# Performance work log

Hardware: AMD Instinct MI355X
Metric: run time of the kernel (lower is better)

Reference implementation:

```python
import jax, jax.numpy as jnp
import numpy as np

N_NODES = 50000
BN_EPS = 1e-5


def graph_conv(x, row, col, ew, n):
    # deg from source indices only (matches torch.bincount(row))
    deg = jnp.zeros((n,), x.dtype).at[row].add(1.0)
    dinv = jnp.where(deg > 0, deg ** -0.5, 0.0)
    norm = dinv[row] * ew * dinv[col]                     # [E]
    msg = norm[:, None] * x[row]                          # [E, F]
    return jax.ops.segment_sum(msg, col, num_segments=n)  # out[dst] += w * x[src]


def batch_norm(x, gamma, beta):
    # training-mode BN over the node (batch) dim, biased variance
    mu = jnp.mean(x, axis=0)
    var = jnp.mean((x - mu) ** 2, axis=0)
    return (x - mu) / jnp.sqrt(var + BN_EPS) * gamma + beta


def setup_inputs() -> dict:
    key = jax.random.key(0)
    ks = jax.random.split(key, 12)
    node_features = jax.random.normal(ks[0], (N_NODES, 100), dtype=jnp.float32)
    edge_index = jax.random.randint(ks[1], (2, 800000), 0, N_NODES, dtype=jnp.int64)
    edge_weights = jax.random.uniform(ks[2], (800000,), dtype=jnp.float32)
    def lin(k, fi, fo):
        lim = 1.0 / np.sqrt(fi)
        k1, k2 = jax.random.split(k)
        W = jax.random.uniform(k1, (fi, fo), minval=-lim, maxval=lim, dtype=jnp.float32)
        b = jax.random.uniform(k2, (fo,), minval=-lim, maxval=lim, dtype=jnp.float32)
        return W, b
    W0, b0 = lin(ks[3], 100, 128)
    W1, b1 = lin(ks[4], 128, 128)
    W2, b2 = lin(ks[5], 128, 64)
    return {
        "node_features": node_features, "edge_index": edge_index, "edge_weights": edge_weights,
        "W0": W0, "b0": b0, "g0": jnp.ones((128,), jnp.float32), "be0": jnp.zeros((128,), jnp.float32),
        "W1": W1, "b1": b1, "g1": jnp.ones((128,), jnp.float32), "be1": jnp.zeros((128,), jnp.float32),
        "W2": W2, "b2": b2,
    }


def reference(node_features, edge_index, edge_weights,
              W0, b0, g0, be0, W1, b1, g1, be1, W2, b2):
    n = node_features.shape[0]
    row, col = edge_index[0], edge_index[1]
    x = node_features
    # layer 0
    x = graph_conv(x, row, col, edge_weights, n)
    x = jax.nn.relu(batch_norm(x @ W0 + b0, g0, be0))
    # layer 1
    x = graph_conv(x, row, col, edge_weights, n)
    x = jax.nn.relu(batch_norm(x @ W1 + b1, g1, be1))
    # final layer (no BN/relu)
    x = graph_conv(x, row, col, edge_weights, n)
    return x @ W2 + b2
```

## Files before the change

### kernel.cpp

```cpp
#include <hip/hip_runtime.h>
#include <cstdint>

#define F0 100
#define FH 128
#define FO 64
#define PD 4
#define BN_EPS 1e-5f

typedef unsigned short ushort_t;
typedef unsigned int uint_t;

static inline int ceil_div(long long a, long long b) { return (int)((a + b - 1) / b); }

__device__ __forceinline__ float bf_lo(uint_t w) { return __uint_as_float(w << 16); }
__device__ __forceinline__ float bf_hi(uint_t w) { return __uint_as_float(w & 0xffff0000u); }
__device__ __forceinline__ uint_t f2bf(float f) {
  uint_t u = __float_as_uint(f);
  return (u + 0x7fffu + ((u >> 16) & 1u)) >> 16;
}
__device__ __forceinline__ uint_t pack2(float a, float b) {
  return f2bf(a) | (f2bf(b) << 16);
}


template <int K, int F, int TM, int BK, bool A_BF16, bool OUT_BF16>
__device__ __forceinline__ void gemm2_body(int bid, const void* __restrict__ A_,
                                           const float* __restrict__ W,
                                           const float* __restrict__ bias,
                                           void* __restrict__ out_, int n) {
  constexpr int NCG = F / 4;
  constexpr int NRG = 256 / NCG;
  constexpr int BR = NRG * TM;
  constexpr int F4 = F / 4;

  __shared__ float sW[BK][F];
  __shared__ float sA[BR][BK];

  const int tid = threadIdx.x;
  const int cg = tid % NCG;
  const int rg = tid / NCG;
  const int row0 = bid * BR;

  float4 acc[TM];
#pragma unroll
  for (int t = 0; t < TM; ++t) acc[t] = make_float4(0.f, 0.f, 0.f, 0.f);

  const float4* W4 = (const float4*)W;
  const float4 z4 = make_float4(0.f, 0.f, 0.f, 0.f);

  for (int k0 = 0; k0 < K; k0 += BK) {
    for (int i = tid; i < BK * F4; i += 256) {
      int kk = i / F4, f4 = i % F4;
      int gk = k0 + kk;
      ((float4*)&sW[kk][0])[f4] = (gk < K) ? W4[(size_t)gk * F4 + f4] : z4;
    }
    for (int i = tid; i < BR * (BK / 4); i += 256) {
      int r = i / (BK / 4), k4 = i % (BK / 4);
      int gr = row0 + r;
      int gk = k0 + k4 * 4;
      float4 av = z4;
      if (gr < n && gk + 3 < K) {
        if (A_BF16) {
          uint2 u = ((const uint2*)A_)[(size_t)gr * (K / 4) + (gk >> 2)];
          av.x = bf_lo(u.x); av.y = bf_hi(u.x);
          av.z = bf_lo(u.y); av.w = bf_hi(u.y);
        } else {
          av = ((const float4*)A_)[(size_t)gr * (K / 4) + (gk >> 2)];
        }
      }
      ((float4*)&sA[r][0])[k4] = av;
    }
    __syncthreads();
#pragma unroll 4
    for (int kk = 0; kk < BK; ++kk) {
      float4 w = ((const float4*)&sW[kk][0])[cg];
#pragma unroll
      for (int t = 0; t < TM; ++t) {
        float a = sA[rg * TM + t][kk];
        acc[t].x = fmaf(a, w.x, acc[t].x);
        acc[t].y = fmaf(a, w.y, acc[t].y);
        acc[t].z = fmaf(a, w.z, acc[t].z);
        acc[t].w = fmaf(a, w.w, acc[t].w);
      }
    }
    __syncthreads();
  }

  float4 bb = bias ? ((const float4*)bias)[cg] : z4;
#pragma unroll
  for (int t = 0; t < TM; ++t) {
    int gr = row0 + rg * TM + t;
    if (gr < n) {
      float4 v = acc[t];
      v.x += bb.x; v.y += bb.y; v.z += bb.z; v.w += bb.w;
      if (OUT_BF16) {
        ((uint2*)out_)[(size_t)gr * F4 + cg] = make_uint2(pack2(v.x, v.y), pack2(v.z, v.w));
      } else {
        ((float4*)out_)[(size_t)gr * F4 + cg] = v;
      }
    }
  }
}


__global__ __launch_bounds__(256) void fused_gemm_hist_kernel(
    const float* __restrict__ A, const float* __restrict__ W, void* __restrict__ out, int n,
    int GB, const int* __restrict__ row, const int* __restrict__ col,
    int* __restrict__ degr_p, int* __restrict__ degc_p, int* __restrict__ posw, int E) {
  int bid = blockIdx.x;
  int r5 = bid % 5;
  int g = bid / 5;
  if (r5 == 0 && g < GB) {
    gemm2_body<F0, FH, 8, 16, false, true>(g, A, W, nullptr, out, n);
    return;
  }
  int h = (r5 == 0) ? (bid - GB) : (bid - (g + 1));
  int e = h * 256 + threadIdx.x;
  if (e >= E) return;
  atomicAdd(&degr_p[(size_t)row[e] * PD], 1);
  posw[e] = atomicAdd(&degc_p[(size_t)col[e] * PD], 1);
}


__global__ __launch_bounds__(256) void scan_fused_kernel(const int* __restrict__ degr_p,
                                                         const int* __restrict__ degc_p,
                                                         float* __restrict__ dinv,
                                                         int* __restrict__ startp,
                                                         int* __restrict__ bsums, int n) {
  __shared__ int s[256];
  int i = blockIdx.x * 256 + threadIdx.x;
  int dc = 0;
  if (i < n) {
    int dr = degr_p[(size_t)i * PD];
    dc = degc_p[(size_t)i * PD];
    dinv[i] = (dr > 0) ? rsqrtf((float)dr) : 0.0f;
  }
  s[threadIdx.x] = dc;
  __syncthreads();
  for (int off = 1; off < 256; off <<= 1) {
    int t = 0;
    if (threadIdx.x >= off) t = s[threadIdx.x - off];
    __syncthreads();
    if (threadIdx.x >= off) s[threadIdx.x] += t;
    __syncthreads();
  }
  if (i < n) startp[i] = s[threadIdx.x] - dc;
  if (threadIdx.x == 255) bsums[blockIdx.x] = s[255];
}

__global__ __launch_bounds__(256) void scan_partials_kernel(int* __restrict__ bsums, int nb) {
  __shared__ int s[256];
  int v = (threadIdx.x < nb) ? bsums[threadIdx.x] : 0;
  s[threadIdx.x] = v;
  __syncthreads();
  for (int off = 1; off < 256; off <<= 1) {
    int t = 0;
    if (threadIdx.x >= off) t = s[threadIdx.x - off];
    __syncthreads();
    if (threadIdx.x >= off) s[threadIdx.x] += t;
    __syncthreads();
  }
  if (threadIdx.x < nb) bsums[threadIdx.x] = s[threadIdx.x] - v;
}


__global__ __launch_bounds__(256) void csr_scatter2_kernel(const int* __restrict__ row,
                                                           const int* __restrict__ col,
                                                           const float* __restrict__ ew,
                                                           const float* __restrict__ dinv,
                                                           const int* __restrict__ startp,
                                                           const int* __restrict__ bsums,
                                                           const int* __restrict__ posw,
                                                           int2* __restrict__ ep, int E) {
  int e = blockIdx.x * blockDim.x + threadIdx.x;
  if (e >= E) return;
  int r = row[e], c = col[e];
  int pos = startp[c] + bsums[c >> 8] + posw[e];
  float coef = dinv[r] * ew[e] * dinv[c];
  ep[pos] = make_int2(r, __float_as_int(coef));
}


template <bool DO_BN>
__device__ __forceinline__ void conv_accum_128(const ushort_t* __restrict__ x, int s0, int d,
                                               int q, const int2* __restrict__ ep,
                                               const float* __restrict__ scale,
                                               const float* __restrict__ shift,
                                               float* __restrict__ acc) {
  constexpr int G2 = FH / 8;
  constexpr int TPD = 8;
  const uint4* x4 = (const uint4*)x;

  float sc[16], sh[16];
  if (DO_BN) {
#pragma unroll
    for (int ch = 0; ch < 2; ++ch) {
      int g = q + ch * TPD;
#pragma unroll
      for (int j = 0; j < 8; ++j) {
        sc[ch * 8 + j] = scale[g * 8 + j];
        sh[ch * 8 + j] = shift[g * 8 + j];
      }
    }
  }
#pragma unroll
  for (int j = 0; j < 16; ++j) acc[j] = 0.f;

  for (int k = 0; k < d; ++k) {
    int2 e = ep[s0 + k];
    float c = __int_as_float(e.y);
    const uint4* xp = x4 + (size_t)e.x * G2 + q;
    uint4 v0 = xp[0];
    uint4 v1 = xp[TPD];
    uint_t vv[8] = {v0.x, v0.y, v0.z, v0.w, v1.x, v1.y, v1.z, v1.w};
#pragma unroll
    for (int hh = 0; hh < 8; ++hh) {
      float f0 = bf_lo(vv[hh]);
      float f1 = bf_hi(vv[hh]);
      if (DO_BN) {
        f0 = fmaxf(fmaf(f0, sc[2 * hh], sh[2 * hh]), 0.f);
        f1 = fmaxf(fmaf(f1, sc[2 * hh + 1], sh[2 * hh + 1]), 0.f);
      }
      acc[2 * hh] = fmaf(c, f0, acc[2 * hh]);
      acc[2 * hh + 1] = fmaf(c, f1, acc[2 * hh + 1]);
    }
  }
}


__global__ __launch_bounds__(256) void conv0_kernel(const ushort_t* __restrict__ x,
                                                    const int* __restrict__ startp,
                                                    const int* __restrict__ bsums,
                                                    const int* __restrict__ degc_p,
                                                    const int2* __restrict__ ep,
                                                    const float* __restrict__ bias,
                                                    ushort_t* __restrict__ out, int n) {
  constexpr int TPD = 8;
  long long tid = (long long)blockIdx.x * 256 + threadIdx.x;
  if (tid >= (long long)n * TPD) return;
  int dst = (int)(tid / TPD);
  int q = (int)(tid % TPD);
  int s0 = startp[dst] + bsums[dst >> 8];
  int d = degc_p[(size_t)dst * PD];
  float acc[16];
  conv_accum_128<false>(x, s0, d, q, ep, nullptr, nullptr, acc);
#pragma unroll
  for (int ch = 0; ch < 2; ++ch) {
    int g = q + ch * TPD;
#pragma unroll
    for (int j = 0; j < 8; ++j) acc[ch * 8 + j] += bias[g * 8 + j];
  }
  uint4* o4 = (uint4*)out;
  size_t base = (size_t)dst * (FH / 8);
  o4[base + q] = make_uint4(pack2(acc[0], acc[1]), pack2(acc[2], acc[3]),
                            pack2(acc[4], acc[5]), pack2(acc[6], acc[7]));
  o4[base + q + TPD] = make_uint4(pack2(acc[8], acc[9]), pack2(acc[10], acc[11]),
                                  pack2(acc[12], acc[13]), pack2(acc[14], acc[15]));
}


template <int FOUT, bool OUT_F32>
__global__ __launch_bounds__(256) void convgemm_kernel(const ushort_t* __restrict__ x,
                                                       const int* __restrict__ startp,
                                                       const int* __restrict__ bsums,
                                                       const int* __restrict__ degc_p,
                                                       const int2* __restrict__ ep,
                                                       const float* __restrict__ scale,
                                                       const float* __restrict__ shift,
                                                       const float* __restrict__ W,
                                                       const float* __restrict__ bias,
                                                       void* __restrict__ out, int n) {
  constexpr int TPD = 8;
  constexpr int BKG = 16;
  constexpr int CPT = FOUT / 8;
  __shared__ float sY[32][FH + 1];
  __shared__ float sW[BKG][FOUT];

  const int tid = threadIdx.x;
  const int dl = tid / TPD;
  const int q = tid % TPD;
  const int dst = blockIdx.x * 32 + dl;
  const bool valid = dst < n;

  float acc[16];
  if (valid) {
    int s0 = startp[dst] + bsums[dst >> 8];
    int d = degc_p[(size_t)dst * PD];
    conv_accum_128<true>(x, s0, d, q, ep, scale, shift, acc);
  } else {
#pragma unroll
    for (int j = 0; j < 16; ++j) acc[j] = 0.f;
  }
#pragma unroll
  for (int j = 0; j < 8; ++j) {
    sY[dl][8 * q + j] = acc[j];
    sY[dl][64 + 8 * q + j] = acc[8 + j];
  }
  __syncthreads();

  const int r = tid / 8;
  const int cg = tid % 8;
  float oacc[CPT];
#pragma unroll
  for (int j = 0; j < CPT; ++j) oacc[j] = 0.f;

  const float4* W4 = (const float4*)W;
  for (int k0 = 0; k0 < FH; k0 += BKG) {
    for (int i = tid; i < BKG * (FOUT / 4); i += 256) {
      int kk = i / (FOUT / 4), f4 = i % (FOUT / 4);
      ((float4*)&sW[kk][0])[f4] = W4[(size_t)(k0 + kk) * (FOUT / 4) + f4];
    }
    __syncthreads();
#pragma unroll 4
    for (int kk = 0; kk < BKG; ++kk) {
      float a = sY[r][k0 + kk];
      const float* wrow = &sW[kk][cg * CPT];
#pragma unroll
      for (int j = 0; j < CPT; ++j) oacc[j] = fmaf(a, wrow[j], oacc[j]);
    }
    __syncthreads();
  }

  int gr = blockIdx.x * 32 + r;
  if (gr >= n) return;
#pragma unroll
  for (int j = 0; j < CPT; ++j) oacc[j] += bias[cg * CPT + j];

  if (OUT_F32) {
    float4* o4 = (float4*)out;
    size_t base = (size_t)gr * (FOUT / 4) + cg * (CPT / 4);
#pragma unroll
    for (int j = 0; j < CPT / 4; ++j)
      o4[base + j] = make_float4(oacc[4 * j], oacc[4 * j + 1], oacc[4 * j + 2], oacc[4 * j + 3]);
  } else {
    uint2* o2 = (uint2*)out;
    size_t base = (size_t)gr * (FOUT / 4) + cg * (CPT / 4);
#pragma unroll
    for (int j = 0; j < CPT / 4; ++j)
      o2[base + j] = make_uint2(pack2(oacc[4 * j], oacc[4 * j + 1]),
                                pack2(oacc[4 * j + 2], oacc[4 * j + 3]));
  }
}


__global__ __launch_bounds__(128) void bn_stats_fin_kernel(const ushort_t* __restrict__ z,
                                                           float* __restrict__ sum,
                                                           float* __restrict__ sumsq,
                                                           const float* __restrict__ g,
                                                           const float* __restrict__ be,
                                                           float* __restrict__ scale,
                                                           float* __restrict__ shift,
                                                           int n, int* __restrict__ ctr) {
  int f = threadIdx.x;
  float s = 0.0f, s2 = 0.0f;
  for (int r = blockIdx.x; r < n; r += gridDim.x) {
    float v = __uint_as_float(((uint_t)z[(size_t)r * FH + f]) << 16);
    s += v;
    s2 += v * v;
  }
  unsafeAtomicAdd(&sum[f], s);
  unsafeAtomicAdd(&sumsq[f], s2);
  __threadfence();
  __syncthreads();
  __shared__ int lastFlag;
  if (f == 0) lastFlag = (atomicAdd(ctr, 1) == (int)gridDim.x - 1) ? 1 : 0;
  __syncthreads();
  if (lastFlag) {
    float S = atomicAdd(&sum[f], 0.0f);
    float S2 = atomicAdd(&sumsq[f], 0.0f);
    float invN = 1.0f / (float)n;
    float mean = S * invN;
    float var = fmaxf(S2 * invN - mean * mean, 0.0f);
    float sc = g[f] / sqrtf(var + BN_EPS);
    scale[f] = sc;
    shift[f] = be[f] - mean * sc;
  }
}


extern "C" void kernel_launch(void* const* d_in, const int* in_sizes, int n_in,
                              void* d_out, int out_size, void* d_ws, size_t ws_size,
                              hipStream_t stream) {
  const float* x   = (const float*)d_in[0];
  const int*   ei  = (const int*)d_in[1];
  const float* ew  = (const float*)d_in[2];
  const float* W0  = (const float*)d_in[3];
  const float* b0  = (const float*)d_in[4];
  const float* g0  = (const float*)d_in[5];
  const float* be0 = (const float*)d_in[6];
  const float* W1  = (const float*)d_in[7];
  const float* b1  = (const float*)d_in[8];
  const float* g1  = (const float*)d_in[9];
  const float* be1 = (const float*)d_in[10];
  const float* W2  = (const float*)d_in[11];
  const float* b2  = (const float*)d_in[12];

  const int n = in_sizes[0] / F0;
  const int E = in_sizes[2];
  const int* row = ei;
  const int* col = ei + E;

  ushort_t* bufA  = (ushort_t*)d_ws;
  ushort_t* bufB  = bufA + (size_t)n * FH;
  int2*   ep      = (int2*)(bufB + (size_t)n * FH);
  int*    degc_p  = (int*)(ep + E);
  int*    degr_p  = degc_p + (size_t)n * PD;
  float*  sum0    = (float*)(degr_p + (size_t)n * PD);
  float*  sumsq0  = sum0 + FH;
  float*  sum1    = sumsq0 + FH;
  float*  sumsq1  = sum1 + FH;
  int*    ctr     = (int*)(sumsq1 + FH);
  const size_t zero_bytes = (2 * (size_t)n * PD + 4 * FH + 2) * 4;
  int*    startp  = ctr + 2;
  float*  dinv    = (float*)(startp + n);
  int*    bsums   = (int*)(dinv + n);
  float*  scale0  = (float*)(bsums + 256);
  float*  shift0  = scale0 + FH;
  float*  scale1  = shift0 + FH;
  float*  shift1  = scale1 + FH;
  int*    posw    = (int*)bufB;

  const int nb = ceil_div(n, 256);
  const int GB = ceil_div(n, 64);
  const int HB = ceil_div(E, 256);
  const int CB = ceil_div(n, 32);

  (void)hipMemsetAsync(degc_p, 0, zero_bytes, stream);
  fused_gemm_hist_kernel<<<GB + HB, 256, 0, stream>>>(x, W0, bufA, n, GB, row, col,
                                                      degr_p, degc_p, posw, E);
  scan_fused_kernel<<<nb, 256, 0, stream>>>(degr_p, degc_p, dinv, startp, bsums, n);
  scan_partials_kernel<<<1, 256, 0, stream>>>(bsums, nb);
  csr_scatter2_kernel<<<HB, 256, 0, stream>>>(row, col, ew, dinv, startp, bsums, posw, ep, E);

  conv0_kernel<<<CB, 256, 0, stream>>>(bufA, startp, bsums, degc_p, ep, b0, bufB, n);
  bn_stats_fin_kernel<<<256, 128, 0, stream>>>(bufB, sum0, sumsq0, g0, be0, scale0, shift0,
                                               n, ctr + 0);
  convgemm_kernel<FH, false><<<CB, 256, 0, stream>>>(bufB, startp, bsums, degc_p, ep,
                                                     scale0, shift0, W1, b1, bufA, n);
  bn_stats_fin_kernel<<<256, 128, 0, stream>>>(bufA, sum1, sumsq1, g1, be1, scale1, shift1,
                                               n, ctr + 1);
  convgemm_kernel<FO, true><<<CB, 256, 0, stream>>>(bufA, startp, bsums, degc_p, ep,
                                                    scale1, shift1, W2, b2, (float*)d_out, n);
}
```

Before: 409.7 us.

## Unfuse conv+GEMM, reorder final layer to GEMM-then-conv, fuse scan passes

The fused conv+GEMM kernels are split into a standalone CSR aggregation kernel and a tiled GEMM kernel. The last layer now applies W2 before aggregation, so it gathers 64-wide rows instead of 128-wide ones, with the BN1 scale/shift and ReLU folded into the GEMM's A-tile load. The separate scan-partials kernel is folded into the scan kernel using a last-block counter, and BN statistics now use 16-byte loads with a shared-memory reduction. This adds launches and bf16 intermediate round trips through memory in exchange for cheaper gathers and better GEMM tiling. The extra bf16 rounding of the intermediates is a precision risk.

```diff
diff --git a/kernel.cpp b/kernel.cpp
--- a/kernel.cpp
+++ b/kernel.cpp
@@ -23,10 +23,12 @@
 }
 
 
-template <int K, int F, int TM, int BK, bool A_BF16, bool OUT_BF16>
+template <int K, int F, int TM, int BK, bool BN_A, bool A_BF16, bool OUT_BF16>
 __device__ __forceinline__ void gemm2_body(int bid, const void* __restrict__ A_,
                                            const float* __restrict__ W,
                                            const float* __restrict__ bias,
+                                           const float* __restrict__ scA,
+                                           const float* __restrict__ shA,
                                            void* __restrict__ out_, int n) {
   constexpr int NCG = F / 4;
   constexpr int NRG = 256 / NCG;
@@ -67,6 +69,14 @@
         } else {
           av = ((const float4*)A_)[(size_t)gr * (K / 4) + (gk >> 2)];
         }
+        if (BN_A) {
+          float4 sc = ((const float4*)scA)[gk >> 2];
+          float4 sh = ((const float4*)shA)[gk >> 2];
+          av.x = fmaxf(fmaf(av.x, sc.x, sh.x), 0.f);
+          av.y = fmaxf(fmaf(av.y, sc.y, sh.y), 0.f);
+          av.z = fmaxf(fmaf(av.z, sc.z, sh.z), 0.f);
+          av.w = fmaxf(fmaf(av.w, sc.w, sh.w), 0.f);
+        }
       }
       ((float4*)&sA[r][0])[k4] = av;
     }
@@ -102,6 +112,16 @@
   }
 }
 
+template <int K, int F, int TM, int BK, bool BN_A, bool A_BF16, bool OUT_BF16>
+__global__ __launch_bounds__(256) void gemm2_kernel(const void* __restrict__ A,
+                                                    const float* __restrict__ W,
+                                                    const float* __restrict__ bias,
+                                                    const float* __restrict__ scA,
+                                                    const float* __restrict__ shA,
+                                                    void* __restrict__ out, int n) {
+  gemm2_body<K, F, TM, BK, BN_A, A_BF16, OUT_BF16>(blockIdx.x, A, W, bias, scA, shA, out, n);
+}
+
 
 __global__ __launch_bounds__(256) void fused_gemm_hist_kernel(
     const float* __restrict__ A, const float* __restrict__ W, void* __restrict__ out, int n,
@@ -111,7 +131,7 @@
   int r5 = bid % 5;
   int g = bid / 5;
   if (r5 == 0 && g < GB) {
-    gemm2_body<F0, FH, 8, 16, false, true>(g, A, W, nullptr, out, n);
+    gemm2_body<F0, FH, 8, 16, false, false, true>(g, A, W, nullptr, nullptr, nullptr, out, n);
     return;
   }
   int h = (r5 == 0) ? (bid - GB) : (bid - (g + 1));
@@ -126,41 +146,46 @@
                                                          const int* __restrict__ degc_p,
                                                          float* __restrict__ dinv,
                                                          int* __restrict__ startp,
-                                                         int* __restrict__ bsums, int n) {
+                                                         int* __restrict__ bsums, int n,
+                                                         int* __restrict__ ctr) {
   __shared__ int s[256];
-  int i = blockIdx.x * 256 + threadIdx.x;
+  const int tid = threadIdx.x;
+  int i = blockIdx.x * 256 + tid;
   int dc = 0;
   if (i < n) {
     int dr = degr_p[(size_t)i * PD];
     dc = degc_p[(size_t)i * PD];
     dinv[i] = (dr > 0) ? rsqrtf((float)dr) : 0.0f;
   }
-  s[threadIdx.x] = dc;
+  s[tid] = dc;
   __syncthreads();
   for (int off = 1; off < 256; off <<= 1) {
     int t = 0;
-    if (threadIdx.x >= off) t = s[threadIdx.x - off];
-    __syncthreads();
-    if (threadIdx.x >= off) s[threadIdx.x] += t;
-    __syncthreads();
-  }
-  if (i < n) startp[i] = s[threadIdx.x] - dc;
-  if (threadIdx.x == 255) bsums[blockIdx.x] = s[255];
-}
-
-__global__ __launch_bounds__(256) void scan_partials_kernel(int* __restrict__ bsums, int nb) {
-  __shared__ int s[256];
-  int v = (threadIdx.x < nb) ? bsums[threadIdx.x] : 0;
-  s[threadIdx.x] = v;
+    if (tid >= off) t = s[tid - off];
+    __syncthreads();
+    if (tid >= off) s[tid] += t;
+    __syncthreads();
+  }
+  if (i < n) startp[i] = s[tid] - dc;
+  if (tid == 255) bsums[blockIdx.x] = s[255];
+  __threadfence();
+  __syncthreads();
+  __shared__ int lastFlag;
+  if (tid == 0) lastFlag = (atomicAdd(ctr, 1) == (int)gridDim.x - 1) ? 1 : 0;
+  __syncthreads();
+  if (!lastFlag) return;
+  int nb = (int)gridDim.x;
+  int v = (tid < nb) ? atomicAdd(&bsums[tid], 0) : 0;
+  s[tid] = v;
   __syncthreads();
   for (int off = 1; off < 256; off <<= 1) {
     int t = 0;
-    if (threadIdx.x >= off) t = s[threadIdx.x - off];
-    __syncthreads();
-    if (threadIdx.x >= off) s[threadIdx.x] += t;
-    __syncthreads();
-  }
-  if (threadIdx.x < nb) bsums[threadIdx.x] = s[threadIdx.x] - v;
+    if (tid >= off) t = s[tid - off];
+    __syncthreads();
+    if (tid >= off) s[tid] += t;
+    __syncthreads();
+  }
+  if (tid < nb) bsums[tid] = s[tid] - v;
 }
 
 
@@ -181,14 +206,24 @@
 }
 
 
-template <bool DO_BN>
-__device__ __forceinline__ void conv_accum_128(const ushort_t* __restrict__ x, int s0, int d,
-                                               int q, const int2* __restrict__ ep,
-                                               const float* __restrict__ scale,
-                                               const float* __restrict__ shift,
-                                               float* __restrict__ acc) {
-  constexpr int G2 = FH / 8;
-  constexpr int TPD = 8;
+template <int F, bool DO_BN, bool OUT_F32>
+__global__ __launch_bounds__(256) void conv_kernel(const ushort_t* __restrict__ x,
+                                                   const int* __restrict__ startp,
+                                                   const int* __restrict__ bsums,
+                                                   const int* __restrict__ degc_p,
+                                                   const int2* __restrict__ ep,
+                                                   const float* __restrict__ bias,
+                                                   const float* __restrict__ scale,
+                                                   const float* __restrict__ shift,
+                                                   void* __restrict__ out, int n) {
+  constexpr int G2 = F / 8;
+  constexpr int TPD = G2 / 2;
+  long long tid = (long long)blockIdx.x * 256 + threadIdx.x;
+  if (tid >= (long long)n * TPD) return;
+  int dst = (int)(tid / TPD);
+  int q = (int)(tid % TPD);
+  int s0 = startp[dst] + bsums[dst >> 8];
+  int d = degc_p[(size_t)dst * PD];
   const uint4* x4 = (const uint4*)x;
 
   float sc[16], sh[16];
@@ -203,6 +238,8 @@
       }
     }
   }
+
+  float acc[16];
 #pragma unroll
   for (int j = 0; j < 16; ++j) acc[j] = 0.f;
 
@@ -225,155 +262,107 @@
       acc[2 * hh + 1] = fmaf(c, f1, acc[2 * hh + 1]);
     }
   }
-}
-
-
-__global__ __launch_bounds__(256) void conv0_kernel(const ushort_t* __restrict__ x,
-                                                    const int* __restrict__ startp,
-                                                    const int* __restrict__ bsums,
-                                                    const int* __restrict__ degc_p,
-                                                    const int2* __restrict__ ep,
-                                                    const float* __restrict__ bias,
-                                                    ushort_t* __restrict__ out, int n) {
-  constexpr int TPD = 8;
-  long long tid = (long long)blockIdx.x * 256 + threadIdx.x;
-  if (tid >= (long long)n * TPD) return;
-  int dst = (int)(tid / TPD);
-  int q = (int)(tid % TPD);
-  int s0 = startp[dst] + bsums[dst >> 8];
-  int d = degc_p[(size_t)dst * PD];
-  float acc[16];
-  conv_accum_128<false>(x, s0, d, q, ep, nullptr, nullptr, acc);
-#pragma unroll
-  for (int ch = 0; ch < 2; ++ch) {
-    int g = q + ch * TPD;
-#pragma unroll
-    for (int j = 0; j < 8; ++j) acc[ch * 8 + j] += bias[g * 8 + j];
-  }
-  uint4* o4 = (uint4*)out;
-  size_t base = (size_t)dst * (FH / 8);
-  o4[base + q] = make_uint4(pack2(acc[0], acc[1]), pack2(acc[2], acc[3]),
-                            pack2(acc[4], acc[5]), pack2(acc[6], acc[7]));
-  o4[base + q + TPD] = make_uint4(pack2(acc[8], acc[9]), pack2(acc[10], acc[11]),
-                                  pack2(acc[12], acc[13]), pack2(acc[14], acc[15]));
-}
-
-
-template <int FOUT, bool OUT_F32>
-__global__ __launch_bounds__(256) void convgemm_kernel(const ushort_t* __restrict__ x,
-                                                       const int* __restrict__ startp,
-                                                       const int* __restrict__ bsums,
-                                                       const int* __restrict__ degc_p,
-                                                       const int2* __restrict__ ep,
-                                                       const float* __restrict__ scale,
-                                                       const float* __restrict__ shift,
-                                                       const float* __restrict__ W,
-                                                       const float* __restrict__ bias,
-                                                       void* __restrict__ out, int n) {
-  constexpr int TPD = 8;
-  constexpr int BKG = 16;
-  constexpr int CPT = FOUT / 8;
-  __shared__ float sY[32][FH + 1];
-  __shared__ float sW[BKG][FOUT];
-
-  const int tid = threadIdx.x;
-  const int dl = tid / TPD;
-  const int q = tid % TPD;
-  const int dst = blockIdx.x * 32 + dl;
-  const bool valid = dst < n;
-
-  float acc[16];
-  if (valid) {
-    int s0 = startp[dst] + bsums[dst >> 8];
-    int d = degc_p[(size_t)dst * PD];
-    conv_accum_128<true>(x, s0, d, q, ep, scale, shift, acc);
-  } else {
-#pragma unroll
-    for (int j = 0; j < 16; ++j) acc[j] = 0.f;
-  }
-#pragma unroll
-  for (int j = 0; j < 8; ++j) {
-    sY[dl][8 * q + j] = acc[j];
-    sY[dl][64 + 8 * q + j] = acc[8 + j];
-  }
-  __syncthreads();
-
-  const int r = tid / 8;
-  const int cg = tid % 8;
-  float oacc[CPT];
-#pragma unroll
-  for (int j = 0; j < CPT; ++j) oacc[j] = 0.f;
-
-  const float4* W4 = (const float4*)W;
-  for (int k0 = 0; k0 < FH; k0 += BKG) {
-    for (int i = tid; i < BKG * (FOUT / 4); i += 256) {
-      int kk = i / (FOUT / 4), f4 = i % (FOUT / 4);
-      ((float4*)&sW[kk][0])[f4] = W4[(size_t)(k0 + kk) * (FOUT / 4) + f4];
-    }
-    __syncthreads();
-#pragma unroll 4
-    for (int kk = 0; kk < BKG; ++kk) {
-      float a = sY[r][k0 + kk];
-      const float* wrow = &sW[kk][cg * CPT];
-#pragma unroll
-      for (int j = 0; j < CPT; ++j) oacc[j] = fmaf(a, wrow[j], oacc[j]);
-    }
-    __syncthreads();
-  }
-
-  int gr = blockIdx.x * 32 + r;
-  if (gr >= n) return;
-#pragma unroll
-  for (int j = 0; j < CPT; ++j) oacc[j] += bias[cg * CPT + j];
+
+  if (bias) {
+#pragma unroll
+    for (int ch = 0; ch < 2; ++ch) {
+      int g = q + ch * TPD;
+#pragma unroll
+      for (int j = 0; j < 8; ++j) acc[ch * 8 + j] += bias[g * 8 + j];
+    }
+  }
 
   if (OUT_F32) {
     float4* o4 = (float4*)out;
-    size_t base = (size_t)gr * (FOUT / 4) + cg * (CPT / 4);
-#pragma unroll
-    for (int j = 0; j < CPT / 4; ++j)
-      o4[base + j] = make_float4(oacc[4 * j], oacc[4 * j + 1], oacc[4 * j + 2], oacc[4 * j + 3]);
+    size_t base = (size_t)dst * (F / 4);
+    o4[base + 2 * q] = make_float4(acc[0], acc[1], acc[2], acc[3]);
+    o4[base + 2 * q + 1] = make_float4(acc[4], acc[5], acc[6], acc[7]);
+    o4[base + 2 * (q + TPD)] = make_float4(acc[8], acc[9], acc[10], acc[11]);
+    o4[base + 2 * (q + TPD) + 1] = make_float4(acc[12], acc[13], acc[14], acc[15]);
   } else {
-    uint2* o2 = (uint2*)out;
-    size_t base = (size_t)gr * (FOUT / 4) + cg * (CPT / 4);
-#pragma unroll
-    for (int j = 0; j < CPT / 4; ++j)
-      o2[base + j] = make_uint2(pack2(oacc[4 * j], oacc[4 * j + 1]),
-                                pack2(oacc[4 * j + 2], oacc[4 * j + 3]));
-  }
-}
-
-
-__global__ __launch_bounds__(128) void bn_stats_fin_kernel(const ushort_t* __restrict__ z,
-                                                           float* __restrict__ sum,
-                                                           float* __restrict__ sumsq,
-                                                           const float* __restrict__ g,
-                                                           const float* __restrict__ be,
-                                                           float* __restrict__ scale,
-                                                           float* __restrict__ shift,
-                                                           int n, int* __restrict__ ctr) {
-  int f = threadIdx.x;
-  float s = 0.0f, s2 = 0.0f;
-  for (int r = blockIdx.x; r < n; r += gridDim.x) {
-    float v = __uint_as_float(((uint_t)z[(size_t)r * FH + f]) << 16);
-    s += v;
-    s2 += v * v;
-  }
-  unsafeAtomicAdd(&sum[f], s);
-  unsafeAtomicAdd(&sumsq[f], s2);
+    uint4* o4 = (uint4*)out;
+    size_t base = (size_t)dst * G2;
+    o4[base + q] = make_uint4(pack2(acc[0], acc[1]), pack2(acc[2], acc[3]),
+                              pack2(acc[4], acc[5]), pack2(acc[6], acc[7]));
+    o4[base + q + TPD] = make_uint4(pack2(acc[8], acc[9]), pack2(acc[10], acc[11]),
+                                    pack2(acc[12], acc[13]), pack2(acc[14], acc[15]));
+  }
+}
+
+
+__global__ __launch_bounds__(256) void bn_stats_fast_kernel(const ushort_t* __restrict__ z,
+                                                            float* __restrict__ sum,
+                                                            float* __restrict__ sumsq,
+                                                            const float* __restrict__ g,
+                                                            const float* __restrict__ be,
+                                                            float* __restrict__ scale,
+                                                            float* __restrict__ shift,
+                                                            int n, int* __restrict__ ctr) {
+  const int tid = threadIdx.x;
+  const int q = tid & 15;
+  const int rg = tid >> 4;
+  const uint4* z4 = (const uint4*)z;
+
+  float s[8], s2[8];
+#pragma unroll
+  for (int j = 0; j < 8; ++j) { s[j] = 0.f; s2[j] = 0.f; }
+
+  for (int r = blockIdx.x * 16 + rg; r < n; r += (int)gridDim.x * 16) {
+    uint4 v = z4[(size_t)r * (FH / 8) + q];
+    uint_t vv[4] = {v.x, v.y, v.z, v.w};
+#pragma unroll
+    for (int h = 0; h < 4; ++h) {
+      float f0 = bf_lo(vv[h]);
+      float f1 = bf_hi(vv[h]);
+      s[2 * h] += f0;      s2[2 * h] += f0 * f0;
+      s[2 * h + 1] += f1;  s2[2 * h + 1] += f1 * f1;
+    }
+  }
+
+  __shared__ float red[256][8];
+#pragma unroll
+  for (int j = 0; j < 8; ++j) red[tid][j] = s[j];
+  __syncthreads();
+  for (int off = 128; off >= 16; off >>= 1) {
+    if (tid < off) {
+#pragma unroll
+      for (int j = 0; j < 8; ++j) red[tid][j] += red[tid + off][j];
+    }
+    __syncthreads();
+  }
+  if (tid < 16) {
+#pragma unroll
+    for (int j = 0; j < 8; ++j) unsafeAtomicAdd(&sum[8 * tid + j], red[tid][j]);
+  }
+  __syncthreads();
+#pragma unroll
+  for (int j = 0; j < 8; ++j) red[tid][j] = s2[j];
+  __syncthreads();
+  for (int off = 128; off >= 16; off >>= 1) {
+    if (tid < off) {
+#pragma unroll
+      for (int j = 0; j < 8; ++j) red[tid][j] += red[tid + off][j];
+    }
+    __syncthreads();
+  }
+  if (tid < 16) {
+#pragma unroll
+    for (int j = 0; j < 8; ++j) unsafeAtomicAdd(&sumsq[8 * tid + j], red[tid][j]);
+  }
   __threadfence();
   __syncthreads();
   __shared__ int lastFlag;
-  if (f == 0) lastFlag = (atomicAdd(ctr, 1) == (int)gridDim.x - 1) ? 1 : 0;
-  __syncthreads();
-  if (lastFlag) {
-    float S = atomicAdd(&sum[f], 0.0f);
-    float S2 = atomicAdd(&sumsq[f], 0.0f);
+  if (tid == 0) lastFlag = (atomicAdd(ctr, 1) == (int)gridDim.x - 1) ? 1 : 0;
+  __syncthreads();
+  if (lastFlag && tid < FH) {
+    float S = atomicAdd(&sum[tid], 0.0f);
+    float S2 = atomicAdd(&sumsq[tid], 0.0f);
     float invN = 1.0f / (float)n;
     float mean = S * invN;
     float var = fmaxf(S2 * invN - mean * mean, 0.0f);
-    float sc = g[f] / sqrtf(var + BN_EPS);
-    scale[f] = sc;
-    shift[f] = be[f] - mean * sc;
+    float sc = g[tid] / sqrtf(var + BN_EPS);
+    scale[tid] = sc;
+    shift[tid] = be[tid] - mean * sc;
   }
 }
 
@@ -410,8 +399,8 @@
   float*  sum1    = sumsq0 + FH;
   float*  sumsq1  = sum1 + FH;
   int*    ctr     = (int*)(sumsq1 + FH);
-  const size_t zero_bytes = (2 * (size_t)n * PD + 4 * FH + 2) * 4;
-  int*    startp  = ctr + 2;
+  const size_t zero_bytes = (2 * (size_t)n * PD + 4 * FH + 3) * 4;
+  int*    startp  = ctr + 3;
   float*  dinv    = (float*)(startp + n);
   int*    bsums   = (int*)(dinv + n);
   float*  scale0  = (float*)(bsums + 256);
@@ -423,22 +412,26 @@
   const int nb = ceil_div(n, 256);
   const int GB = ceil_div(n, 64);
   const int HB = ceil_div(E, 256);
-  const int CB = ceil_div(n, 32);
+  const int CB_H = ceil_div((long long)n * (FH / 16), 256);
+  const int CB_O = ceil_div((long long)n * (FO / 16), 256);
 
   (void)hipMemsetAsync(degc_p, 0, zero_bytes, stream);
   fused_gemm_hist_kernel<<<GB + HB, 256, 0, stream>>>(x, W0, bufA, n, GB, row, col,
                                                       degr_p, degc_p, posw, E);
-  scan_fused_kernel<<<nb, 256, 0, stream>>>(degr_p, degc_p, dinv, startp, bsums, n);
-  scan_partials_kernel<<<1, 256, 0, stream>>>(bsums, nb);
+  scan_fused_kernel<<<nb, 256, 0, stream>>>(degr_p, degc_p, dinv, startp, bsums, n, ctr + 0);
   csr_scatter2_kernel<<<HB, 256, 0, stream>>>(row, col, ew, dinv, startp, bsums, posw, ep, E);
-
-  conv0_kernel<<<CB, 256, 0, stream>>>(bufA, startp, bsums, degc_p, ep, b0, bufB, n);
-  bn_stats_fin_kernel<<<256, 128, 0, stream>>>(bufB, sum0, sumsq0, g0, be0, scale0, shift0,
-                                               n, ctr + 0);
-  convgemm_kernel<FH, false><<<CB, 256, 0, stream>>>(bufB, startp, bsums, degc_p, ep,
-                                                     scale0, shift0, W1, b1, bufA, n);
-  bn_stats_fin_kernel<<<256, 128, 0, stream>>>(bufA, sum1, sumsq1, g1, be1, scale1, shift1,
-                                               n, ctr + 1);
-  convgemm_kernel<FO, true><<<CB, 256, 0, stream>>>(bufA, startp, bsums, degc_p, ep,
-                                                    scale1, shift1, W2, b2, (float*)d_out, n);
-}
+  conv_kernel<FH, false, false><<<CB_H, 256, 0, stream>>>(
+      bufA, startp, bsums, degc_p, ep, b0, nullptr, nullptr, bufB, n);
+  bn_stats_fast_kernel<<<128, 256, 0, stream>>>(bufB, sum0, sumsq0, g0, be0, scale0, shift0,
+                                                n, ctr + 1);
+  conv_kernel<FH, true, false><<<CB_H, 256, 0, stream>>>(
+      bufB, startp, bsums, degc_p, ep, nullptr, scale0, shift0, bufA, n);
+  gemm2_kernel<FH, FH, 8, 32, false, true, true><<<GB, 256, 0, stream>>>(
+      bufA, W1, b1, nullptr, nullptr, bufB, n);
+  bn_stats_fast_kernel<<<128, 256, 0, stream>>>(bufB, sum1, sumsq1, g1, be1, scale1, shift1,
+                                                n, ctr + 2);
+  gemm2_kernel<FH, FO, 4, 32, true, true, true><<<GB, 256, 0, stream>>>(
+      bufB, W2, nullptr, scale1, shift1, bufA, n);
+  conv_kernel<FO, false, true><<<CB_O, 256, 0, stream>>>(
+      bufA, startp, bsums, degc_p, ep, b2, nullptr, nullptr, (float*)d_out, n);
+}
```

Result: faster. 367.4 us (-10.3%).
